# Optimization experiments

Measured on AMD Instinct MI355X. Metric: run time of the kernel, lower is better.

## Reference

```python
import jax, jax.numpy as jnp
import numpy as np

NUM_GRAPHS = 512
BN_EPS = 1e-5

def _lin(k, fin, fout):
    kw, kb = jax.random.split(k)
    s = 1.0 / np.sqrt(fin)
    return (jax.random.uniform(kw, (fin, fout), jnp.float32, -s, s),
            jax.random.uniform(kb, (fout,), jnp.float32, -s, s))

def setup_inputs() -> dict:
    key = jax.random.key(0)
    ks = jax.random.split(key, 16)
    N, E, F, C, H, O = 50000, 800000, 128, 256, 512, 768
    x = jax.random.normal(ks[0], (N, F), jnp.float32)
    edge_index = jax.random.randint(ks[1], (2, E), 0, N, jnp.int64)
    batch = jnp.sort(jax.random.randint(ks[2], (N,), 0, NUM_GRAPHS, jnp.int64))
    d = {"x": x, "edge_index": edge_index, "batch": batch}
    d["w1a"], d["b1a"] = _lin(ks[3], F, C)
    d["g1"], d["be1"] = jnp.ones((C,), jnp.float32), jnp.zeros((C,), jnp.float32)
    d["w1b"], d["b1b"] = _lin(ks[4], C, C)
    d["w2a"], d["b2a"] = _lin(ks[5], C, C)
    d["g2"], d["be2"] = jnp.ones((C,), jnp.float32), jnp.zeros((C,), jnp.float32)
    d["w2b"], d["b2b"] = _lin(ks[6], C, C)
    d["w3a"], d["b3a"] = _lin(ks[7], C, C)
    d["g3"], d["be3"] = jnp.ones((C,), jnp.float32), jnp.zeros((C,), jnp.float32)
    d["w3b"], d["b3b"] = _lin(ks[8], C, C)
    d["wh1"], d["bh1"] = _lin(ks[9], C, H)
    d["wh2"], d["bh2"] = _lin(ks[10], H, O)
    return d

def _bn(z, g, b):
    mu = jnp.mean(z, axis=0)
    var = jnp.mean((z - mu) ** 2, axis=0)  # biased var, torch BN training mode
    return (z - mu) * jax.lax.rsqrt(var + BN_EPS) * g + b

def _gin(x, edge_index, wa, ba, g, be, wb, bb, tanh_out):
    src, dst = edge_index[0], edge_index[1]
    agg = jax.ops.segment_sum(x[src], dst, num_segments=x.shape[0])
    h = x + agg  # eps = 0
    z = jax.nn.relu(_bn(h @ wa + ba, g, be))
    z = z @ wb + bb
    return jnp.tanh(z) if tanh_out else z

def reference(x, edge_index, batch,
              w1a, b1a, g1, be1, w1b, b1b,
              w2a, b2a, g2, be2, w2b, b2b,
              w3a, b3a, g3, be3, w3b, b3b,
              wh1, bh1, wh2, bh2):
    h = jax.nn.relu(_gin(x, edge_index, w1a, b1a, g1, be1, w1b, b1b, False))
    h = jax.nn.relu(_gin(h, edge_index, w2a, b2a, g2, be2, w2b, b2b, True))
    h = _gin(h, edge_index, w3a, b3a, g3, be3, w3b, b3b, True)
    # global mean pool over graphs
    sums = jax.ops.segment_sum(h, batch, num_segments=NUM_GRAPHS)
    cnt = jax.ops.segment_sum(jnp.ones((h.shape[0],), h.dtype), batch, num_segments=NUM_GRAPHS)
    pooled = sums / jnp.maximum(cnt, 1.0)[:, None]
    z = jax.nn.relu(pooled @ wh1 + bh1)
    return z @ wh2 + bh2
```

## Files before the change

kernel.cpp:

```cpp
#include <hip/hip_runtime.h>


typedef __attribute__((ext_vector_type(8))) short short8;
typedef __attribute__((ext_vector_type(4))) float f32x4;
typedef __attribute__((ext_vector_type(4))) unsigned short us4;
typedef __attribute__((ext_vector_type(8))) unsigned short us8;

__device__ __forceinline__ unsigned short f2bf(float f) {
  unsigned int b = __float_as_uint(f);
  unsigned int r = 0x7FFFu + ((b >> 16) & 1u);
  return (unsigned short)((b + r) >> 16);
}
__device__ __forceinline__ float bf2f(unsigned short u) {
  return __uint_as_float(((unsigned int)u) << 16);
}

__device__ __forceinline__ int swv(int row) {
  return (row & 3) ^ ((row >> 2) & 3);
}

typedef const __attribute__((address_space(1))) unsigned int* gas1;
typedef __attribute__((address_space(3))) unsigned int* las3;
__device__ __forceinline__ void gload16(const void* g, void* l) {
  __builtin_amdgcn_global_load_lds((gas1)g, (las3)l, 16, 0, 0);
}

__device__ __forceinline__ size_t swz4_idx(int row, int k, int K) {
  int g = k >> 3;
  return (size_t)row * K + ((g >> 2) << 5) + ((((g & 3) ^ swv(row)) << 3)) + (k & 7);
}

__global__ void k_histbounds(const int* __restrict__ ei, int* __restrict__ deg, int E,
                             int eb, const int* __restrict__ batch,
                             int* __restrict__ gs, int* __restrict__ ge, int N) {
  int b = blockIdx.x;
  if (b < eb) {
    int e = b * 256 + threadIdx.x;
    if (e < E) atomicAdd(&deg[ei[E + e]], 1);
  } else {
    int i = (b - eb) * 256 + threadIdx.x;
    if (i < N) {
      int bb = batch[i];
      if (i == 0 || batch[i - 1] != bb) gs[bb] = i;
      if (i == N - 1 || batch[i + 1] != bb) ge[bb] = i + 1;
    }
  }
}

__global__ __launch_bounds__(1024) void k_scan1(const int* __restrict__ deg,
                                                int* __restrict__ partial,
                                                int* __restrict__ bsum, int N) {
  __shared__ int sd[1024];
  int tid = threadIdx.x;
  int i = blockIdx.x * 1024 + tid;
  int v = (i < N) ? deg[i] : 0;
  sd[tid] = v;
  __syncthreads();
  for (int off = 1; off < 1024; off <<= 1) {
    int t = (tid >= off) ? sd[tid - off] : 0;
    __syncthreads();
    sd[tid] += t;
    __syncthreads();
  }
  if (i < N) partial[i] = sd[tid];
  if (tid == 1023) bsum[blockIdx.x] = sd[1023];
}

__global__ void k_scan2(int* __restrict__ bsum, int nb) {
  int l = threadIdx.x;
  int orig = (l < nb) ? bsum[l] : 0;
  int v = orig;
  for (int off = 1; off < 64; off <<= 1) {
    int t = __shfl_up(v, off);
    if (l >= off) v += t;
  }
  if (l < nb) bsum[l] = v - orig;
}

__global__ void k_scan3(const int* __restrict__ deg, const int* __restrict__ partial,
                        const int* __restrict__ bsum, int* __restrict__ rowptr,
                        int* __restrict__ cursor, int N) {
  int i = blockIdx.x * 256 + threadIdx.x;
  if (i >= N) return;
  int incl = partial[i] + bsum[i >> 10];
  rowptr[i + 1] = incl;
  cursor[i] = incl - deg[i];
  if (i == 0) rowptr[0] = 0;
}

__global__ void k_fill(const int* __restrict__ ei, int* __restrict__ cursor,
                       int* __restrict__ adj, int E) {
  int e = blockIdx.x * 256 + threadIdx.x;
  if (e >= E) return;
  int s = ei[e];
  int d = ei[E + e];
  int pos = atomicAdd(&cursor[d], 1);
  adj[pos] = s;
}

__global__ void k_xbf(const float* __restrict__ X, unsigned short* __restrict__ Xb,
                      int total) {
  int t = blockIdx.x * 256 + threadIdx.x;
  if (t * 8 >= total) return;
  const float4 v0 = *(const float4*)(X + t * 8);
  const float4 v1 = *(const float4*)(X + t * 8 + 4);
  us8 o;
  o[0] = f2bf(v0.x); o[1] = f2bf(v0.y); o[2] = f2bf(v0.z); o[3] = f2bf(v0.w);
  o[4] = f2bf(v1.x); o[5] = f2bf(v1.y); o[6] = f2bf(v1.z); o[7] = f2bf(v1.w);
  *(us8*)(Xb + t * 8) = o;
}

__global__ void k_prep_all(const float* __restrict__ w1a, const float* __restrict__ w1b,
                           const float* __restrict__ w2a, const float* __restrict__ w2b,
                           const float* __restrict__ w3a, const float* __restrict__ w3b,
                           const float* __restrict__ wh1, const float* __restrict__ wh2,
                           unsigned short* __restrict__ Hi, unsigned short* __restrict__ Lo) {
  int idx = blockIdx.x * 256 + threadIdx.x;
  const float* W; int K, Nout, lo_;
  if (idx < 32768)       { W = w1a; K = 128; Nout = 256; lo_ = 0; }
  else if (idx < 98304)  { W = w1b; K = 256; Nout = 256; lo_ = 32768; }
  else if (idx < 163840) { W = w2a; K = 256; Nout = 256; lo_ = 98304; }
  else if (idx < 229376) { W = w2b; K = 256; Nout = 256; lo_ = 163840; }
  else if (idx < 294912) { W = w3a; K = 256; Nout = 256; lo_ = 229376; }
  else if (idx < 360448) { W = w3b; K = 256; Nout = 256; lo_ = 294912; }
  else if (idx < 491520) { W = wh1; K = 256; Nout = 512; lo_ = 360448; }
  else                   { W = wh2; K = 512; Nout = 768; lo_ = 491520; }
  int li = idx - lo_;
  int n = li % Nout, k = li / Nout;
  float w = W[k * Nout + n];
  unsigned short h = f2bf(w);
  size_t oi = (size_t)lo_ + swz4_idx(n, k, K);
  Hi[oi] = h;
  Lo[oi] = f2bf(w - bf2f(h));
}

template <int C>
__global__ __launch_bounds__(256) void k_agg(const unsigned short* __restrict__ Xb,
                                             unsigned short* __restrict__ Hb,
                                             const int* __restrict__ rowptr,
                                             const int* __restrict__ adj, int N,
                                             float* __restrict__ statsZ) {
  if (blockIdx.x == 0) {
    statsZ[threadIdx.x] = 0.f;
    statsZ[256 + threadIdx.x] = 0.f;
  }
  int node = blockIdx.x * 4 + (threadIdx.x >> 6);
  if (node >= N) return;
  int lane = threadIdx.x & 63;
  int e0 = rowptr[node], e1 = rowptr[node + 1];
  if constexpr (C == 256) {
    us4 ov = *(const us4*)(Xb + (size_t)node * C + lane * 4);
    float a0 = bf2f(ov[0]), a1 = bf2f(ov[1]), a2 = bf2f(ov[2]), a3 = bf2f(ov[3]);
    int e = e0;
    for (; e + 4 <= e1; e += 4) {
      int s0 = adj[e], s1 = adj[e + 1], s2 = adj[e + 2], s3 = adj[e + 3];
      us4 v0 = *(const us4*)(Xb + (size_t)s0 * C + lane * 4);
      us4 v1 = *(const us4*)(Xb + (size_t)s1 * C + lane * 4);
      us4 v2 = *(const us4*)(Xb + (size_t)s2 * C + lane * 4);
      us4 v3 = *(const us4*)(Xb + (size_t)s3 * C + lane * 4);
      a0 += (bf2f(v0[0]) + bf2f(v1[0])) + (bf2f(v2[0]) + bf2f(v3[0]));
      a1 += (bf2f(v0[1]) + bf2f(v1[1])) + (bf2f(v2[1]) + bf2f(v3[1]));
      a2 += (bf2f(v0[2]) + bf2f(v1[2])) + (bf2f(v2[2]) + bf2f(v3[2]));
      a3 += (bf2f(v0[3]) + bf2f(v1[3])) + (bf2f(v2[3]) + bf2f(v3[3]));
    }
    for (; e < e1; ++e) {
      us4 v = *(const us4*)(Xb + (size_t)adj[e] * C + lane * 4);
      a0 += bf2f(v[0]); a1 += bf2f(v[1]); a2 += bf2f(v[2]); a3 += bf2f(v[3]);
    }
    us4 hv;
    hv[0] = f2bf(a0); hv[1] = f2bf(a1); hv[2] = f2bf(a2); hv[3] = f2bf(a3);
    size_t oi = (size_t)node * 256 + ((lane >> 3) << 5) +
                ((((lane >> 1) & 3) ^ swv(node)) << 3) + ((lane & 1) << 2);
    *(us4*)(Hb + oi) = hv;
  } else {
    ushort2 ov = *(const ushort2*)(Xb + (size_t)node * C + lane * 2);
    float a0 = bf2f(ov.x), a1 = bf2f(ov.y);
    int e = e0;
    for (; e + 4 <= e1; e += 4) {
      int s0 = adj[e], s1 = adj[e + 1], s2 = adj[e + 2], s3 = adj[e + 3];
      ushort2 v0 = *(const ushort2*)(Xb + (size_t)s0 * C + lane * 2);
      ushort2 v1 = *(const ushort2*)(Xb + (size_t)s1 * C + lane * 2);
      ushort2 v2 = *(const ushort2*)(Xb + (size_t)s2 * C + lane * 2);
      ushort2 v3 = *(const ushort2*)(Xb + (size_t)s3 * C + lane * 2);
      a0 += (bf2f(v0.x) + bf2f(v1.x)) + (bf2f(v2.x) + bf2f(v3.x));
      a1 += (bf2f(v0.y) + bf2f(v1.y)) + (bf2f(v2.y) + bf2f(v3.y));
    }
    for (; e < e1; ++e) {
      ushort2 v = *(const ushort2*)(Xb + (size_t)adj[e] * C + lane * 2);
      a0 += bf2f(v.x); a1 += bf2f(v.y);
    }
    ushort2 hv = {f2bf(a0), f2bf(a1)};
    size_t oi = (size_t)node * 128 + ((lane >> 4) << 5) +
                ((((lane >> 2) & 3) ^ swv(node)) << 3) + ((lane & 3) << 1);
    *(ushort2*)(Hb + oi) = hv;
  }
}

template <int EPI, bool STATS, bool OSPLIT, bool XSWZ, int ASRC, bool FULL, bool OBF16>
__global__ __launch_bounds__(256) void k_gemm(
    const unsigned short* __restrict__ AHb, const unsigned short* __restrict__ ALo,
    const unsigned short* __restrict__ Zb,
    int M, int K, int Nld, int mb, int per,
    const unsigned short* __restrict__ WHi, const unsigned short* __restrict__ WLo,
    const float* __restrict__ bias,
    const float* __restrict__ statsIn, const float* __restrict__ gvec,
    const float* __restrict__ bevec,
    float* __restrict__ Out, unsigned short* __restrict__ OutB,
    unsigned short* __restrict__ OHi, unsigned short* __restrict__ OLo,
    float* __restrict__ statsOut) {
  __shared__ unsigned short aHi[2048], bHi[4096];
  __shared__ unsigned short aLo[FULL ? 2048 : 64], bLo[FULL ? 4096 : 64];
  __shared__ float sBNsc[ASRC == 2 ? 256 : 1], sBNsh[ASRC == 2 ? 256 : 1];
  int bx, by;
  if constexpr (XSWZ) {
    int xcd = blockIdx.x & 7, slot = blockIdx.x >> 3;
    bx = xcd * per + (slot >> 1);
    by = slot & 1;
    if (bx >= mb) return;
  } else {
    bx = blockIdx.x;
    by = blockIdx.y;
  }
  const int tid = threadIdx.x;
  const int lane = tid & 63, w = tid >> 6;
  const int wm = w >> 1, wn = w & 1;
  const int m0 = bx * 64, n0 = by * 128;

  if constexpr (ASRC == 2) {
    float mu = statsIn[tid] / (float)M;
    float var = statsIn[256 + tid] / (float)M - mu * mu;
    float sc = gvec[tid] * rsqrtf(var + 1e-5f);
    sBNsc[tid] = sc;
    sBNsh[tid] = bevec[tid] - mu * sc;
  }

  f32x4 zero = {0.f, 0.f, 0.f, 0.f};
  f32x4 acc[2][4];
#pragma unroll
  for (int i = 0; i < 2; ++i)
#pragma unroll
    for (int j = 0; j < 4; ++j) acc[i][j] = zero;

  const int rq = lane >> 2;
  const int k8s = lane & 3;

  us8 zr;
  const unsigned short* zbase0 = nullptr;
  if constexpr (ASRC == 2) {
    int row0 = tid >> 2, gq0 = tid & 3;
    int ra0 = m0 + row0; if (ra0 >= M) ra0 = M - 1;
    zbase0 = Zb + (size_t)ra0 * K + gq0 * 8;
    zr = *(const us8*)(zbase0);
  }

  for (int kb = 0; kb < K; kb += 32) {
    __syncthreads();
    if constexpr (ASRC == 2) {
      int row = tid >> 2, gq = tid & 3;
      us8 hv;
#pragma unroll
      for (int jj = 0; jj < 8; ++jj) {
        int kc = kb + gq * 8 + jj;
        float o = fmaxf(bf2f(zr[jj]) * sBNsc[kc] + sBNsh[kc], 0.f);
        hv[jj] = f2bf(o);
      }
      int bo = row * 64 + ((gq ^ swv(row)) << 4);
      *(us8*)((char*)aHi + bo) = hv;
#pragma unroll
      for (int q = 0; q < 2; ++q) {
        int rloc = (w << 5) + (q << 4) + rq;
        size_t gb = (size_t)(n0 + rloc) * K + kb + k8s * 8;
        unsigned bo2 = (w << 11) + (q << 10);
        gload16(WHi + gb, (char*)bHi + bo2);
      }
    } else {
      int raA = m0 + (w << 4) + rq; if (raA >= M) raA = M - 1;
      size_t ga = (size_t)raA * K + kb + k8s * 8;
      gload16(AHb + ga, (char*)aHi + (w << 10));
      if constexpr (FULL) gload16(ALo + ga, (char*)aLo + (w << 10));
#pragma unroll
      for (int q = 0; q < 2; ++q) {
        int rloc = (w << 5) + (q << 4) + rq;
        size_t gb = (size_t)(n0 + rloc) * K + kb + k8s * 8;
        unsigned bo2 = (w << 11) + (q << 10);
        gload16(WHi + gb, (char*)bHi + bo2);
        if constexpr (FULL) gload16(WLo + gb, (char*)bLo + bo2);
      }
    }
    __syncthreads();

    if constexpr (ASRC == 2) {
      if (kb + 32 < K) zr = *(const us8*)(zbase0 + kb + 32);
    }

    const int j = lane >> 4;
    short8 bh[4], bl[4];
#pragma unroll
    for (int ni = 0; ni < 4; ++ni) {
      int r = wn * 64 + ni * 16 + (lane & 15);
      int bo = r * 64 + ((j ^ swv(r)) << 4);
      bh[ni] = *(const short8*)((const char*)bHi + bo);
      if constexpr (FULL) bl[ni] = *(const short8*)((const char*)bLo + bo);
    }
#pragma unroll
    for (int mi = 0; mi < 2; ++mi) {
      int r = wm * 32 + mi * 16 + (lane & 15);
      int bo = r * 64 + ((j ^ swv(r)) << 4);
      short8 ah = *(const short8*)((const char*)aHi + bo);
#pragma unroll
      for (int ni = 0; ni < 4; ++ni) {
        acc[mi][ni] = __builtin_amdgcn_mfma_f32_16x16x32_bf16(ah, bh[ni], acc[mi][ni], 0, 0, 0);
        if constexpr (FULL) {
          short8 al = *(const short8*)((const char*)aLo + bo);
          acc[mi][ni] = __builtin_amdgcn_mfma_f32_16x16x32_bf16(ah, bl[ni], acc[mi][ni], 0, 0, 0);
          acc[mi][ni] = __builtin_amdgcn_mfma_f32_16x16x32_bf16(al, bh[ni], acc[mi][ni], 0, 0, 0);
        }
      }
    }
  }

#pragma unroll
  for (int ni = 0; ni < 4; ++ni) {
    int col = n0 + wn * 64 + ni * 16 + (lane & 15);
    float bc = bias[col];
    float s = 0.f, q = 0.f;
#pragma unroll
    for (int mi = 0; mi < 2; ++mi) {
      int rbase = m0 + wm * 32 + mi * 16 + (lane >> 4) * 4;
#pragma unroll
      for (int r = 0; r < 4; ++r) {
        int row = rbase + r;
        if (row < M) {
          float o = acc[mi][ni][r] + bc;
          if (STATS) { s += o; q += o * o; }
          if (OSPLIT) {
            o = fmaxf(o, 0.f);
            unsigned short h = f2bf(o);
            size_t oi = swz4_idx(row, col, Nld);
            OHi[oi] = h;
            OLo[oi] = f2bf(o - bf2f(h));
          } else {
            if (EPI == 1) o = fmaxf(o, 0.f);
            else if (EPI == 2) o = tanhf(o);
            else if (EPI == 3) o = fmaxf(tanhf(o), 0.f);
            if (OBF16) OutB[(size_t)row * Nld + col] = f2bf(o);
            else       Out[(size_t)row * Nld + col] = o;
          }
        }
      }
    }
    if (STATS) {
      s += __shfl_xor(s, 16); s += __shfl_xor(s, 32);
      q += __shfl_xor(q, 16); q += __shfl_xor(q, 32);
      if ((lane >> 4) == 0) {
        atomicAdd(&statsOut[col], s);
        atomicAdd(&statsOut[256 + col], q);
      }
    }
  }
}

__global__ __launch_bounds__(256) void k_pool(const unsigned short* __restrict__ Hb,
                                              const int* __restrict__ gs,
                                              const int* __restrict__ ge,
                                              unsigned short* __restrict__ PHi,
                                              unsigned short* __restrict__ PLo) {
  __shared__ float4 red[4][64];
  int gi = blockIdx.x;
  int s = gs[gi], e = ge[gi];
  int w = threadIdx.x >> 6, lane = threadIdx.x & 63;
  float4 acc = {0.f, 0.f, 0.f, 0.f};
  for (int r = s + w; r < e; r += 4) {
    us4 v = *(const us4*)(Hb + (size_t)r * 256 + lane * 4);
    acc.x += bf2f(v[0]); acc.y += bf2f(v[1]);
    acc.z += bf2f(v[2]); acc.w += bf2f(v[3]);
  }
  red[w][lane] = acc;
  __syncthreads();
  if (w == 0) {
    float4 a = red[0][lane], b = red[1][lane], c = red[2][lane], d = red[3][lane];
    float inv = 1.0f / fmaxf((float)(e - s), 1.0f);
    float vv[4] = {(a.x + b.x + c.x + d.x) * inv, (a.y + b.y + c.y + d.y) * inv,
                   (a.z + b.z + c.z + d.z) * inv, (a.w + b.w + c.w + d.w) * inv};
    us4 hv, lv;
#pragma unroll
    for (int j = 0; j < 4; ++j) {
      unsigned short h = f2bf(vv[j]);
      hv[j] = h;
      lv[j] = f2bf(vv[j] - bf2f(h));
    }
    size_t oi = (size_t)gi * 256 + ((lane >> 3) << 5) +
                ((((lane >> 1) & 3) ^ swv(gi)) << 3) + ((lane & 1) << 2);
    *(us4*)(PHi + oi) = hv;
    *(us4*)(PLo + oi) = lv;
  }
}

extern "C" void kernel_launch(void* const* d_in, const int* in_sizes, int n_in,
                              void* d_out, int out_size, void* d_ws, size_t ws_size,
                              hipStream_t stream) {
  const float* x      = (const float*)d_in[0];
  const int* ei       = (const int*)d_in[1];
  const int* bat      = (const int*)d_in[2];
  const float* w1a = (const float*)d_in[3];  const float* b1a = (const float*)d_in[4];
  const float* g1  = (const float*)d_in[5];  const float* be1 = (const float*)d_in[6];
  const float* w1b = (const float*)d_in[7];  const float* b1b = (const float*)d_in[8];
  const float* w2a = (const float*)d_in[9];  const float* b2a = (const float*)d_in[10];
  const float* g2  = (const float*)d_in[11]; const float* be2 = (const float*)d_in[12];
  const float* w2b = (const float*)d_in[13]; const float* b2b = (const float*)d_in[14];
  const float* w3a = (const float*)d_in[15]; const float* b3a = (const float*)d_in[16];
  const float* g3  = (const float*)d_in[17]; const float* be3 = (const float*)d_in[18];
  const float* w3b = (const float*)d_in[19]; const float* b3b = (const float*)d_in[20];
  const float* wh1 = (const float*)d_in[21]; const float* bh1 = (const float*)d_in[22];
  const float* wh2 = (const float*)d_in[23]; const float* bh2 = (const float*)d_in[24];
  float* out = (float*)d_out;

  const int N = in_sizes[0] / 128;
  const int E = in_sizes[1] / 2;
  const int G = 512;

  char* ws = (char*)d_ws;
  size_t off = 0;
  auto alloc = [&](size_t bytes) {
    void* p = ws + off;
    off = (off + bytes + 255) & ~(size_t)255;
    return p;
  };
  unsigned short* hb = (unsigned short*)alloc((size_t)N * 256 * 2);
  unsigned short* zb = (unsigned short*)alloc((size_t)N * 256 * 2);
  unsigned short* ab = (unsigned short*)alloc((size_t)N * 256 * 2);
  unsigned short* xb = (unsigned short*)alloc((size_t)N * 128 * 2);
  int* adj     = (int*)alloc((size_t)E * 4);
  int* rowptr  = (int*)alloc((size_t)(N + 1) * 4);
  int* cursor  = (int*)alloc((size_t)N * 4);
  int* deg     = (int*)alloc((size_t)N * 4);
  int* partial = (int*)alloc((size_t)N * 4);
  int* bsum    = (int*)alloc(64 * 4);
  unsigned short* wHi = (unsigned short*)alloc(884736 * 2);
  unsigned short* wLo = (unsigned short*)alloc(884736 * 2);
  float* stats = (float*)alloc(512 * 4);
  int* gs      = (int*)alloc(G * 4);
  int* ge      = (int*)alloc(G * 4);
  unsigned short* poolHi = (unsigned short*)alloc((size_t)G * 256 * 2);
  unsigned short* poolLo = (unsigned short*)alloc((size_t)G * 256 * 2);
  unsigned short* thidHi = (unsigned short*)alloc((size_t)G * 512 * 2);
  unsigned short* thidLo = (unsigned short*)alloc((size_t)G * 512 * 2);

  const int o1a = 0, o1b = 32768, o2a = 98304, o2b = 163840, o3a = 229376, o3b = 294912;
  const int oh1 = 360448, oh2 = 491520;

  hipMemsetAsync(deg, 0, (size_t)N * 4, stream);
  hipMemsetAsync(gs, 0, (size_t)G * 4, stream);
  hipMemsetAsync(ge, 0, (size_t)G * 4, stream);

  int eb = (E + 255) / 256;
  int nbN = (N + 255) / 256;
  int nb1 = (N + 1023) >> 10;
  k_histbounds<<<eb + nbN, 256, 0, stream>>>(ei, deg, E, eb, bat, gs, ge, N);
  k_scan1<<<nb1, 1024, 0, stream>>>(deg, partial, bsum, N);
  k_scan2<<<1, 64, 0, stream>>>(bsum, nb1);
  k_scan3<<<nbN, 256, 0, stream>>>(deg, partial, bsum, rowptr, cursor, N);
  k_fill<<<eb, 256, 0, stream>>>(ei, cursor, adj, E);

  k_xbf<<<(N * 128 / 8 + 255) / 256, 256, 0, stream>>>(x, xb, N * 128);
  k_prep_all<<<3456, 256, 0, stream>>>(w1a, w1b, w2a, w2b, w3a, w3b, wh1, wh2, wHi, wLo);

  int nb4 = (N + 3) / 4;
  const int mb = (N + 63) / 64;
  const int per = (mb + 7) / 8;
  dim3 gg(per * 16);

  k_agg<128><<<nb4, 256, 0, stream>>>(xb, hb, rowptr, adj, N, stats);
  k_gemm<0, true, false, true, 0, false, true><<<gg, 256, 0, stream>>>(
      hb, nullptr, nullptr, N, 128, 256, mb, per, wHi + o1a, wLo + o1a, b1a,
      nullptr, nullptr, nullptr, nullptr, zb, nullptr, nullptr, stats);
  k_gemm<1, false, false, true, 2, false, true><<<gg, 256, 0, stream>>>(
      nullptr, nullptr, zb, N, 256, 256, mb, per, wHi + o1b, wLo + o1b, b1b,
      stats, g1, be1, nullptr, ab, nullptr, nullptr, nullptr);

  k_agg<256><<<nb4, 256, 0, stream>>>(ab, hb, rowptr, adj, N, stats);
  k_gemm<0, true, false, true, 0, false, true><<<gg, 256, 0, stream>>>(
      hb, nullptr, nullptr, N, 256, 256, mb, per, wHi + o2a, wLo + o2a, b2a,
      nullptr, nullptr, nullptr, nullptr, zb, nullptr, nullptr, stats);
  k_gemm<3, false, false, true, 2, false, true><<<gg, 256, 0, stream>>>(
      nullptr, nullptr, zb, N, 256, 256, mb, per, wHi + o2b, wLo + o2b, b2b,
      stats, g2, be2, nullptr, ab, nullptr, nullptr, nullptr);

  k_agg<256><<<nb4, 256, 0, stream>>>(ab, hb, rowptr, adj, N, stats);
  k_gemm<0, true, false, true, 0, false, true><<<gg, 256, 0, stream>>>(
      hb, nullptr, nullptr, N, 256, 256, mb, per, wHi + o3a, wLo + o3a, b3a,
      nullptr, nullptr, nullptr, nullptr, zb, nullptr, nullptr, stats);
  k_gemm<2, false, false, true, 2, false, true><<<gg, 256, 0, stream>>>(
      nullptr, nullptr, zb, N, 256, 256, mb, per, wHi + o3b, wLo + o3b, b3b,
      stats, g3, be3, nullptr, ab, nullptr, nullptr, nullptr);

  k_pool<<<G, 256, 0, stream>>>(ab, gs, ge, poolHi, poolLo);
  dim3 gh1(8, 4);
  k_gemm<1, false, true, false, 0, true, false><<<gh1, 256, 0, stream>>>(
      poolHi, poolLo, nullptr, G, 256, 512, 0, 0, wHi + oh1, wLo + oh1, bh1,
      nullptr, nullptr, nullptr, nullptr, nullptr, thidHi, thidLo, nullptr);
  dim3 gh2(8, 6);
  k_gemm<0, false, false, false, 0, true, false><<<gh2, 256, 0, stream>>>(
      thidHi, thidLo, nullptr, G, 512, 768, 0, 0, wHi + oh2, wLo + oh2, bh2,
      nullptr, nullptr, nullptr, out, nullptr, nullptr, nullptr, nullptr);
}
```

Baseline: 602.3 us.

## Double GEMM K-tile to 64 with 8-way XOR swizzled pre-laid-out operands

Raises the GEMM K step from 32 to 64. The global pre-swizzled layouts of weights, aggregated features and pooled outputs change from a 4-group to an 8-group XOR swizzle to match the wider LDS rows. This halves the number of barrier-separated K iterations and amortizes the load and sync overhead over twice the MFMA work per step. In exchange, LDS use per block doubles and register pressure rises, which can lower occupancy.

```diff
diff --git a/kernel.cpp b/kernel.cpp
--- a/kernel.cpp
+++ b/kernel.cpp
@@ -15,8 +15,8 @@
   return __uint_as_float(((unsigned int)u) << 16);
 }
 
-__device__ __forceinline__ int swv(int row) {
-  return (row & 3) ^ ((row >> 2) & 3);
+__device__ __forceinline__ int sw8(int row) {
+  return (row & 7) ^ ((row >> 3) & 7);
 }
 
 typedef const __attribute__((address_space(1))) unsigned int* gas1;
@@ -25,9 +25,9 @@
   __builtin_amdgcn_global_load_lds((gas1)g, (las3)l, 16, 0, 0);
 }
 
-__device__ __forceinline__ size_t swz4_idx(int row, int k, int K) {
+__device__ __forceinline__ size_t swz8_idx(int row, int k, int K) {
   int g = k >> 3;
-  return (size_t)row * K + ((g >> 2) << 5) + ((((g & 3) ^ swv(row)) << 3)) + (k & 7);
+  return (size_t)row * K + ((g >> 3) << 6) + ((((g & 7) ^ sw8(row)) << 3)) + (k & 7);
 }
 
 __global__ void k_histbounds(const int* __restrict__ ei, int* __restrict__ deg, int E,
@@ -129,7 +129,7 @@
   int n = li % Nout, k = li / Nout;
   float w = W[k * Nout + n];
   unsigned short h = f2bf(w);
-  size_t oi = (size_t)lo_ + swz4_idx(n, k, K);
+  size_t oi = (size_t)lo_ + swz8_idx(n, k, K);
   Hi[oi] = h;
   Lo[oi] = f2bf(w - bf2f(h));
 }
@@ -169,8 +169,8 @@
     }
     us4 hv;
     hv[0] = f2bf(a0); hv[1] = f2bf(a1); hv[2] = f2bf(a2); hv[3] = f2bf(a3);
-    size_t oi = (size_t)node * 256 + ((lane >> 3) << 5) +
-                ((((lane >> 1) & 3) ^ swv(node)) << 3) + ((lane & 1) << 2);
+    size_t oi = (size_t)node * 256 + ((lane >> 4) << 6) +
+                ((((lane >> 1) & 7) ^ sw8(node)) << 3) + ((lane & 1) << 2);
     *(us4*)(Hb + oi) = hv;
   } else {
     ushort2 ov = *(const ushort2*)(Xb + (size_t)node * C + lane * 2);
@@ -190,8 +190,8 @@
       a0 += bf2f(v.x); a1 += bf2f(v.y);
     }
     ushort2 hv = {f2bf(a0), f2bf(a1)};
-    size_t oi = (size_t)node * 128 + ((lane >> 4) << 5) +
-                ((((lane >> 2) & 3) ^ swv(node)) << 3) + ((lane & 3) << 1);
+    size_t oi = (size_t)node * 128 + ((lane >> 5) << 6) +
+                ((((lane >> 2) & 7) ^ sw8(node)) << 3) + ((lane & 3) << 1);
     *(ushort2*)(Hb + oi) = hv;
   }
 }
@@ -208,8 +208,8 @@
     float* __restrict__ Out, unsigned short* __restrict__ OutB,
     unsigned short* __restrict__ OHi, unsigned short* __restrict__ OLo,
     float* __restrict__ statsOut) {
-  __shared__ unsigned short aHi[2048], bHi[4096];
-  __shared__ unsigned short aLo[FULL ? 2048 : 64], bLo[FULL ? 4096 : 64];
+  __shared__ unsigned short aHi[4096], bHi[8192];
+  __shared__ unsigned short aLo[FULL ? 4096 : 64], bLo[FULL ? 8192 : 64];
   __shared__ float sBNsc[ASRC == 2 ? 256 : 1], sBNsh[ASRC == 2 ? 256 : 1];
   int bx, by;
   if constexpr (XSWZ) {
@@ -241,48 +241,61 @@
 #pragma unroll
     for (int j = 0; j < 4; ++j) acc[i][j] = zero;
 
-  const int rq = lane >> 2;
-  const int k8s = lane & 3;
-
-  us8 zr;
-  const unsigned short* zbase0 = nullptr;
+  const int l8 = lane >> 3;
+  const int s8 = lane & 7;
+
+  us8 zr0, zr1;
+  const unsigned short* zb0 = nullptr;
+  const unsigned short* zb1 = nullptr;
   if constexpr (ASRC == 2) {
-    int row0 = tid >> 2, gq0 = tid & 3;
-    int ra0 = m0 + row0; if (ra0 >= M) ra0 = M - 1;
-    zbase0 = Zb + (size_t)ra0 * K + gq0 * 8;
-    zr = *(const us8*)(zbase0);
-  }
-
-  for (int kb = 0; kb < K; kb += 32) {
+    int r0 = tid >> 3, r1 = 32 + (tid >> 3);
+    int ra0 = m0 + r0; if (ra0 >= M) ra0 = M - 1;
+    int ra1 = m0 + r1; if (ra1 >= M) ra1 = M - 1;
+    zb0 = Zb + (size_t)ra0 * K + (tid & 7) * 8;
+    zb1 = Zb + (size_t)ra1 * K + (tid & 7) * 8;
+    zr0 = *(const us8*)(zb0);
+    zr1 = *(const us8*)(zb1);
+  }
+
+  for (int kb = 0; kb < K; kb += 64) {
     __syncthreads();
     if constexpr (ASRC == 2) {
-      int row = tid >> 2, gq = tid & 3;
-      us8 hv;
-#pragma unroll
-      for (int jj = 0; jj < 8; ++jj) {
-        int kc = kb + gq * 8 + jj;
-        float o = fmaxf(bf2f(zr[jj]) * sBNsc[kc] + sBNsh[kc], 0.f);
-        hv[jj] = f2bf(o);
-      }
-      int bo = row * 64 + ((gq ^ swv(row)) << 4);
-      *(us8*)((char*)aHi + bo) = hv;
+#pragma unroll
+      for (int p = 0; p < 2; ++p) {
+        int row = (p << 5) + (tid >> 3), gq = tid & 7;
+        us8 zr = p ? zr1 : zr0;
+        us8 hv;
+#pragma unroll
+        for (int jj = 0; jj < 8; ++jj) {
+          int kc = kb + gq * 8 + jj;
+          float o = fmaxf(bf2f(zr[jj]) * sBNsc[kc] + sBNsh[kc], 0.f);
+          hv[jj] = f2bf(o);
+        }
+        int bo = row * 128 + ((gq ^ sw8(row)) << 4);
+        *(us8*)((char*)aHi + bo) = hv;
+      }
+#pragma unroll
+      for (int q = 0; q < 4; ++q) {
+        int row = (w << 5) + (q << 3) + l8;
+        size_t gb = (size_t)(n0 + row) * K + kb + s8 * 8;
+        unsigned bo2 = (w << 12) + (q << 10);
+        gload16(WHi + gb, (char*)bHi + bo2);
+      }
+    } else {
 #pragma unroll
       for (int q = 0; q < 2; ++q) {
-        int rloc = (w << 5) + (q << 4) + rq;
-        size_t gb = (size_t)(n0 + rloc) * K + kb + k8s * 8;
-        unsigned bo2 = (w << 11) + (q << 10);
-        gload16(WHi + gb, (char*)bHi + bo2);
-      }
-    } else {
-      int raA = m0 + (w << 4) + rq; if (raA >= M) raA = M - 1;
-      size_t ga = (size_t)raA * K + kb + k8s * 8;
-      gload16(AHb + ga, (char*)aHi + (w << 10));
-      if constexpr (FULL) gload16(ALo + ga, (char*)aLo + (w << 10));
-#pragma unroll
-      for (int q = 0; q < 2; ++q) {
-        int rloc = (w << 5) + (q << 4) + rq;
-        size_t gb = (size_t)(n0 + rloc) * K + kb + k8s * 8;
-        unsigned bo2 = (w << 11) + (q << 10);
+        int row = (w << 4) + (q << 3) + l8;
+        int ra = m0 + row; if (ra >= M) ra = M - 1;
+        size_t ga = (size_t)ra * K + kb + s8 * 8;
+        unsigned boA = (w << 11) + (q << 10);
+        gload16(AHb + ga, (char*)aHi + boA);
+        if constexpr (FULL) gload16(ALo + ga, (char*)aLo + boA);
+      }
+#pragma unroll
+      for (int q = 0; q < 4; ++q) {
+        int row = (w << 5) + (q << 3) + l8;
+        size_t gb = (size_t)(n0 + row) * K + kb + s8 * 8;
+        unsigned bo2 = (w << 12) + (q << 10);
         gload16(WHi + gb, (char*)bHi + bo2);
         if constexpr (FULL) gload16(WLo + gb, (char*)bLo + bo2);
       }
@@ -290,30 +303,37 @@
     __syncthreads();
 
     if constexpr (ASRC == 2) {
-      if (kb + 32 < K) zr = *(const us8*)(zbase0 + kb + 32);
+      if (kb + 64 < K) {
+        zr0 = *(const us8*)(zb0 + kb + 64);
+        zr1 = *(const us8*)(zb1 + kb + 64);
+      }
     }
 
     const int j = lane >> 4;
-    short8 bh[4], bl[4];
-#pragma unroll
-    for (int ni = 0; ni < 4; ++ni) {
-      int r = wn * 64 + ni * 16 + (lane & 15);
-      int bo = r * 64 + ((j ^ swv(r)) << 4);
-      bh[ni] = *(const short8*)((const char*)bHi + bo);
-      if constexpr (FULL) bl[ni] = *(const short8*)((const char*)bLo + bo);
-    }
-#pragma unroll
-    for (int mi = 0; mi < 2; ++mi) {
-      int r = wm * 32 + mi * 16 + (lane & 15);
-      int bo = r * 64 + ((j ^ swv(r)) << 4);
-      short8 ah = *(const short8*)((const char*)aHi + bo);
+#pragma unroll
+    for (int kk = 0; kk < 2; ++kk) {
+      int g = (kk << 2) + j;
+      short8 bh[4], bl[4];
 #pragma unroll
       for (int ni = 0; ni < 4; ++ni) {
-        acc[mi][ni] = __builtin_amdgcn_mfma_f32_16x16x32_bf16(ah, bh[ni], acc[mi][ni], 0, 0, 0);
-        if constexpr (FULL) {
-          short8 al = *(const short8*)((const char*)aLo + bo);
-          acc[mi][ni] = __builtin_amdgcn_mfma_f32_16x16x32_bf16(ah, bl[ni], acc[mi][ni], 0, 0, 0);
-          acc[mi][ni] = __builtin_amdgcn_mfma_f32_16x16x32_bf16(al, bh[ni], acc[mi][ni], 0, 0, 0);
+        int r = wn * 64 + ni * 16 + (lane & 15);
+        int bo = r * 128 + ((g ^ sw8(r)) << 4);
+        bh[ni] = *(const short8*)((const char*)bHi + bo);
+        if constexpr (FULL) bl[ni] = *(const short8*)((const char*)bLo + bo);
+      }
+#pragma unroll
+      for (int mi = 0; mi < 2; ++mi) {
+        int r = wm * 32 + mi * 16 + (lane & 15);
+        int bo = r * 128 + ((g ^ sw8(r)) << 4);
+        short8 ah = *(const short8*)((const char*)aHi + bo);
+#pragma unroll
+        for (int ni = 0; ni < 4; ++ni) {
+          acc[mi][ni] = __builtin_amdgcn_mfma_f32_16x16x32_bf16(ah, bh[ni], acc[mi][ni], 0, 0, 0);
+          if constexpr (FULL) {
+            short8 al = *(const short8*)((const char*)aLo + bo);
+            acc[mi][ni] = __builtin_amdgcn_mfma_f32_16x16x32_bf16(ah, bl[ni], acc[mi][ni], 0, 0, 0);
+            acc[mi][ni] = __builtin_amdgcn_mfma_f32_16x16x32_bf16(al, bh[ni], acc[mi][ni], 0, 0, 0);
+          }
         }
       }
     }
@@ -336,7 +356,7 @@
           if (OSPLIT) {
             o = fmaxf(o, 0.f);
             unsigned short h = f2bf(o);
-            size_t oi = swz4_idx(row, col, Nld);
+            size_t oi = swz8_idx(row, col, Nld);
             OHi[oi] = h;
             OLo[oi] = f2bf(o - bf2f(h));
           } else {
@@ -389,8 +409,8 @@
       hv[j] = h;
       lv[j] = f2bf(vv[j] - bf2f(h));
     }
-    size_t oi = (size_t)gi * 256 + ((lane >> 3) << 5) +
-                ((((lane >> 1) & 3) ^ swv(gi)) << 3) + ((lane & 1) << 2);
+    size_t oi = (size_t)gi * 256 + ((lane >> 4) << 6) +
+                ((((lane >> 1) & 7) ^ sw8(gi)) << 3) + ((lane & 1) << 2);
     *(us4*)(PHi + oi) = hv;
     *(us4*)(PLo + oi) = lv;
   }
```

Result: faster. 581.5 us (-3.5%).

## Load GEMM MFMA fragments directly from global memory, drop LDS staging and swizzle

Applied to the files above, without the earlier changes.

Replaces the LDS-staged GEMM main loop, which used global_load_lds into swizzled shared tiles with two barriers per k-step, with direct per-lane 16-byte global loads of the A and B fragments straight into MFMA operands. All producers (weight conversion, aggregation, pooling, split outputs) now write plain row-major layouts instead of the XOR-swizzled layout. This removes LDS traffic and per-iteration synchronisation, but each wave now reloads B from global/L2 with no sharing across waves, and the loads have no software prefetch.

```diff
diff --git a/kernel.cpp b/kernel.cpp
--- a/kernel.cpp
+++ b/kernel.cpp
@@ -13,21 +13,6 @@
 }
 __device__ __forceinline__ float bf2f(unsigned short u) {
   return __uint_as_float(((unsigned int)u) << 16);
-}
-
-__device__ __forceinline__ int swv(int row) {
-  return (row & 3) ^ ((row >> 2) & 3);
-}
-
-typedef const __attribute__((address_space(1))) unsigned int* gas1;
-typedef __attribute__((address_space(3))) unsigned int* las3;
-__device__ __forceinline__ void gload16(const void* g, void* l) {
-  __builtin_amdgcn_global_load_lds((gas1)g, (las3)l, 16, 0, 0);
-}
-
-__device__ __forceinline__ size_t swz4_idx(int row, int k, int K) {
-  int g = k >> 3;
-  return (size_t)row * K + ((g >> 2) << 5) + ((((g & 3) ^ swv(row)) << 3)) + (k & 7);
 }
 
 __global__ void k_histbounds(const int* __restrict__ ei, int* __restrict__ deg, int E,
@@ -129,7 +114,7 @@
   int n = li % Nout, k = li / Nout;
   float w = W[k * Nout + n];
   unsigned short h = f2bf(w);
-  size_t oi = (size_t)lo_ + swz4_idx(n, k, K);
+  size_t oi = (size_t)lo_ + (size_t)n * K + k;
   Hi[oi] = h;
   Lo[oi] = f2bf(w - bf2f(h));
 }
@@ -169,9 +154,7 @@
     }
     us4 hv;
     hv[0] = f2bf(a0); hv[1] = f2bf(a1); hv[2] = f2bf(a2); hv[3] = f2bf(a3);
-    size_t oi = (size_t)node * 256 + ((lane >> 3) << 5) +
-                ((((lane >> 1) & 3) ^ swv(node)) << 3) + ((lane & 1) << 2);
-    *(us4*)(Hb + oi) = hv;
+    *(us4*)(Hb + (size_t)node * C + lane * 4) = hv;
   } else {
     ushort2 ov = *(const ushort2*)(Xb + (size_t)node * C + lane * 2);
     float a0 = bf2f(ov.x), a1 = bf2f(ov.y);
@@ -190,9 +173,7 @@
       a0 += bf2f(v.x); a1 += bf2f(v.y);
     }
     ushort2 hv = {f2bf(a0), f2bf(a1)};
-    size_t oi = (size_t)node * 128 + ((lane >> 4) << 5) +
-                ((((lane >> 2) & 3) ^ swv(node)) << 3) + ((lane & 3) << 1);
-    *(ushort2*)(Hb + oi) = hv;
+    *(ushort2*)(Hb + (size_t)node * C + lane * 2) = hv;
   }
 }
 
@@ -208,8 +189,6 @@
     float* __restrict__ Out, unsigned short* __restrict__ OutB,
     unsigned short* __restrict__ OHi, unsigned short* __restrict__ OLo,
     float* __restrict__ statsOut) {
-  __shared__ unsigned short aHi[2048], bHi[4096];
-  __shared__ unsigned short aLo[FULL ? 2048 : 64], bLo[FULL ? 4096 : 64];
   __shared__ float sBNsc[ASRC == 2 ? 256 : 1], sBNsh[ASRC == 2 ? 256 : 1];
   int bx, by;
   if constexpr (XSWZ) {
@@ -232,6 +211,7 @@
     float sc = gvec[tid] * rsqrtf(var + 1e-5f);
     sBNsc[tid] = sc;
     sBNsh[tid] = bevec[tid] - mu * sc;
+    __syncthreads();
   }
 
   f32x4 zero = {0.f, 0.f, 0.f, 0.f};
@@ -241,81 +221,68 @@
 #pragma unroll
     for (int j = 0; j < 4; ++j) acc[i][j] = zero;
 
-  const int rq = lane >> 2;
-  const int k8s = lane & 3;
-
-  us8 zr;
-  const unsigned short* zbase0 = nullptr;
-  if constexpr (ASRC == 2) {
-    int row0 = tid >> 2, gq0 = tid & 3;
-    int ra0 = m0 + row0; if (ra0 >= M) ra0 = M - 1;
-    zbase0 = Zb + (size_t)ra0 * K + gq0 * 8;
-    zr = *(const us8*)(zbase0);
-  }
+  const int fr = lane & 15;
+  const int fk = (lane >> 4) * 8;
+
+  const unsigned short* asrc = (ASRC == 2) ? Zb : AHb;
+  const unsigned short* ap[2];
+  const unsigned short* bp[4];
+#pragma unroll
+  for (int mi = 0; mi < 2; ++mi) {
+    int ra = m0 + wm * 32 + mi * 16 + fr;
+    if (ra >= M) ra = M - 1;
+    ap[mi] = asrc + (size_t)ra * K + fk;
+  }
+#pragma unroll
+  for (int ni = 0; ni < 4; ++ni)
+    bp[ni] = WHi + (size_t)(n0 + wn * 64 + ni * 16 + fr) * K + fk;
 
   for (int kb = 0; kb < K; kb += 32) {
-    __syncthreads();
+    us8 av[2], bv[4];
+#pragma unroll
+    for (int mi = 0; mi < 2; ++mi) av[mi] = *(const us8*)(ap[mi] + kb);
+#pragma unroll
+    for (int ni = 0; ni < 4; ++ni) bv[ni] = *(const us8*)(bp[ni] + kb);
     if constexpr (ASRC == 2) {
-      int row = tid >> 2, gq = tid & 3;
-      us8 hv;
-#pragma unroll
-      for (int jj = 0; jj < 8; ++jj) {
-        int kc = kb + gq * 8 + jj;
-        float o = fmaxf(bf2f(zr[jj]) * sBNsc[kc] + sBNsh[kc], 0.f);
-        hv[jj] = f2bf(o);
-      }
-      int bo = row * 64 + ((gq ^ swv(row)) << 4);
-      *(us8*)((char*)aHi + bo) = hv;
-#pragma unroll
-      for (int q = 0; q < 2; ++q) {
-        int rloc = (w << 5) + (q << 4) + rq;
-        size_t gb = (size_t)(n0 + rloc) * K + kb + k8s * 8;
-        unsigned bo2 = (w << 11) + (q << 10);
-        gload16(WHi + gb, (char*)bHi + bo2);
-      }
-    } else {
-      int raA = m0 + (w << 4) + rq; if (raA >= M) raA = M - 1;
-      size_t ga = (size_t)raA * K + kb + k8s * 8;
-      gload16(AHb + ga, (char*)aHi + (w << 10));
-      if constexpr (FULL) gload16(ALo + ga, (char*)aLo + (w << 10));
-#pragma unroll
-      for (int q = 0; q < 2; ++q) {
-        int rloc = (w << 5) + (q << 4) + rq;
-        size_t gb = (size_t)(n0 + rloc) * K + kb + k8s * 8;
-        unsigned bo2 = (w << 11) + (q << 10);
-        gload16(WHi + gb, (char*)bHi + bo2);
-        if constexpr (FULL) gload16(WLo + gb, (char*)bLo + bo2);
-      }
-    }
-    __syncthreads();
-
-    if constexpr (ASRC == 2) {
-      if (kb + 32 < K) zr = *(const us8*)(zbase0 + kb + 32);
-    }
-
-    const int j = lane >> 4;
-    short8 bh[4], bl[4];
-#pragma unroll
-    for (int ni = 0; ni < 4; ++ni) {
-      int r = wn * 64 + ni * 16 + (lane & 15);
-      int bo = r * 64 + ((j ^ swv(r)) << 4);
-      bh[ni] = *(const short8*)((const char*)bHi + bo);
-      if constexpr (FULL) bl[ni] = *(const short8*)((const char*)bLo + bo);
-    }
-#pragma unroll
-    for (int mi = 0; mi < 2; ++mi) {
-      int r = wm * 32 + mi * 16 + (lane & 15);
-      int bo = r * 64 + ((j ^ swv(r)) << 4);
-      short8 ah = *(const short8*)((const char*)aHi + bo);
-#pragma unroll
-      for (int ni = 0; ni < 4; ++ni) {
-        acc[mi][ni] = __builtin_amdgcn_mfma_f32_16x16x32_bf16(ah, bh[ni], acc[mi][ni], 0, 0, 0);
-        if constexpr (FULL) {
-          short8 al = *(const short8*)((const char*)aLo + bo);
-          acc[mi][ni] = __builtin_amdgcn_mfma_f32_16x16x32_bf16(ah, bl[ni], acc[mi][ni], 0, 0, 0);
-          acc[mi][ni] = __builtin_amdgcn_mfma_f32_16x16x32_bf16(al, bh[ni], acc[mi][ni], 0, 0, 0);
+#pragma unroll
+      for (int mi = 0; mi < 2; ++mi) {
+#pragma unroll
+        for (int jj = 0; jj < 8; ++jj) {
+          int kc = kb + fk + jj;
+          float o = fmaxf(bf2f(av[mi][jj]) * sBNsc[kc] + sBNsh[kc], 0.f);
+          av[mi][jj] = f2bf(o);
         }
       }
+    }
+    if constexpr (FULL) {
+      us8 al[2], bl[4];
+#pragma unroll
+      for (int mi = 0; mi < 2; ++mi) {
+        int ra = m0 + wm * 32 + mi * 16 + fr;
+        if (ra >= M) ra = M - 1;
+        al[mi] = *(const us8*)(ALo + (size_t)ra * K + fk + kb);
+      }
+#pragma unroll
+      for (int ni = 0; ni < 4; ++ni)
+        bl[ni] = *(const us8*)(WLo + (size_t)(n0 + wn * 64 + ni * 16 + fr) * K + fk + kb);
+#pragma unroll
+      for (int mi = 0; mi < 2; ++mi)
+#pragma unroll
+        for (int ni = 0; ni < 4; ++ni) {
+          acc[mi][ni] = __builtin_amdgcn_mfma_f32_16x16x32_bf16(
+              (short8)av[mi], (short8)bv[ni], acc[mi][ni], 0, 0, 0);
+          acc[mi][ni] = __builtin_amdgcn_mfma_f32_16x16x32_bf16(
+              (short8)av[mi], (short8)bl[ni], acc[mi][ni], 0, 0, 0);
+          acc[mi][ni] = __builtin_amdgcn_mfma_f32_16x16x32_bf16(
+              (short8)al[mi], (short8)bv[ni], acc[mi][ni], 0, 0, 0);
+        }
+    } else {
+#pragma unroll
+      for (int mi = 0; mi < 2; ++mi)
+#pragma unroll
+        for (int ni = 0; ni < 4; ++ni)
+          acc[mi][ni] = __builtin_amdgcn_mfma_f32_16x16x32_bf16(
+              (short8)av[mi], (short8)bv[ni], acc[mi][ni], 0, 0, 0);
     }
   }
 
@@ -336,7 +303,7 @@
           if (OSPLIT) {
             o = fmaxf(o, 0.f);
             unsigned short h = f2bf(o);
-            size_t oi = swz4_idx(row, col, Nld);
+            size_t oi = (size_t)row * Nld + col;
             OHi[oi] = h;
             OLo[oi] = f2bf(o - bf2f(h));
           } else {
@@ -389,10 +356,8 @@
       hv[j] = h;
       lv[j] = f2bf(vv[j] - bf2f(h));
     }
-    size_t oi = (size_t)gi * 256 + ((lane >> 3) << 5) +
-                ((((lane >> 1) & 3) ^ swv(gi)) << 3) + ((lane & 1) << 2);
-    *(us4*)(PHi + oi) = hv;
-    *(us4*)(PLo + oi) = lv;
+    *(us4*)(PHi + (size_t)gi * 256 + lane * 4) = hv;
+    *(us4*)(PLo + (size_t)gi * 256 + lane * 4) = lv;
   }
 }
 
```

After: 714.1 us. +18.5%, slower.
